# Performance work log

Measured on AMD Instinct MI355X. Metric: run time of the kernel, lower is better.

## Reference

```python
import jax, jax.numpy as jnp
import numpy as np
from jax import lax
from jax.scipy.special import logsumexp

NUM_CLASSES = 170
ALPHA = 0.2
B, T = 16, 8192


def setup_inputs() -> dict:
    key = jax.random.key(0)
    logits = jax.random.normal(key, (B, T, NUM_CLASSES), dtype=jnp.float32)
    # transition matrix: alpha on diagonal, uniform off-diagonal
    off = (1.0 - ALPHA) / (NUM_CLASSES - 1)
    trans = jnp.full((NUM_CLASSES, NUM_CLASSES), off, dtype=jnp.float32)
    trans = trans.at[jnp.arange(NUM_CLASSES), jnp.arange(NUM_CLASSES)].set(ALPHA)
    init = jnp.full((NUM_CLASSES,), 1.0 / NUM_CLASSES, dtype=jnp.float32)
    return {"logits": logits, "transition_matrix": trans, "initial_distribution": init}


def reference(logits, transition_matrix, initial_distribution):
    eps = 1e-12
    log_T = jnp.log(transition_matrix + eps)          # (C, C)
    log_init = jnp.log(initial_distribution + eps)    # (C,)
    log_probs = jax.nn.log_softmax(logits, axis=-1)   # (B, T, C)
    Bn, Tn, C = log_probs.shape
    lp = jnp.moveaxis(log_probs, 1, 0)                # (T, B, C) time-major for scan

    # forward recursion: alpha_t[j] = logsumexp_i(alpha_{t-1}[i] + logT[i,j]) + lp_t[j]
    alpha0 = log_init[None, :] + lp[0]                # (B, C)

    def fwd_step(a_prev, lp_t):
        a = logsumexp(a_prev[:, :, None] + log_T[None, :, :], axis=1) + lp_t
        return a, a

    _, alpha_rest = lax.scan(fwd_step, alpha0, lp[1:])
    alpha = jnp.concatenate([alpha0[None], alpha_rest], axis=0)  # (T, B, C)

    # backward recursion: beta_t[i] = logsumexp_j(logT[i,j] + lp_{t+1}[j] + beta_{t+1}[j])
    betaT = jnp.zeros((Bn, C), dtype=log_probs.dtype)

    def bwd_step(b_next, lp_next):
        b = logsumexp(log_T[None, :, :] + (lp_next + b_next)[:, None, :], axis=2)
        return b, b

    _, beta_rest = lax.scan(bwd_step, betaT, lp[1:], reverse=True)
    beta = jnp.concatenate([beta_rest, betaT[None]], axis=0)     # (T, B, C)

    posterior = jax.nn.softmax(alpha + beta, axis=-1)            # (T, B, C)
    return jnp.moveaxis(posterior, 0, 1)                         # (B, T, C)
```

## Files before the change

kernel.cpp:

```cpp
#include <hip/hip_runtime.h>
#include <hip/hip_fp16.h>


#define NCLS 170
#define BB 16
#define TT 8192
#define LCH 16
#define WARM 16
#define NCHUNK (TT / LCH)

typedef float f32x2 __attribute__((ext_vector_type(2)));

struct Row { f32x2 xy; float z; };

__device__ __forceinline__ float wave_sum_b(float x) {
  x += __int_as_float(__builtin_amdgcn_update_dpp(0, __float_as_int(x), 0x111, 0xF, 0xF, true));
  x += __int_as_float(__builtin_amdgcn_update_dpp(0, __float_as_int(x), 0x112, 0xF, 0xF, true));
  x += __int_as_float(__builtin_amdgcn_update_dpp(0, __float_as_int(x), 0x114, 0xF, 0xF, true));
  x += __int_as_float(__builtin_amdgcn_update_dpp(0, __float_as_int(x), 0x118, 0xF, 0xF, true));
  x += __int_as_float(__builtin_amdgcn_update_dpp(0, __float_as_int(x), 0x142, 0xA, 0xF, true));
  x += __int_as_float(__builtin_amdgcn_update_dpp(0, __float_as_int(x), 0x143, 0xC, 0xF, true));
  return __int_as_float(__builtin_amdgcn_readlane(__float_as_int(x), 63));
}

__global__ __launch_bounds__(256, 2) void hmm_fb(const float* __restrict__ logits,
                                                 const float* __restrict__ trans,
                                                 const float* __restrict__ initd,
                                                 float* __restrict__ out) {
  __shared__ __half2 pb01[4 * LCH * 64];
  const int lane = threadIdx.x & 63;
  const int w = threadIdx.x >> 6;
  __half2* pw = pb01 + w * (LCH * 64);

  const int d = blockIdx.x;
  const int o = (d & 7) * (BB * NCHUNK / 32) + (d >> 3);
  const int g = o * 4 + w;
  const int b = g / NCHUNK;
  const int chunk = g % NCHUNK;
  const int t0 = chunk * LCH;
  const int t1 = t0 + LCH;

  const float off = trans[1] + 1e-12f;
  const float dia = trans[0] + 1e-12f;
  const float dd = dia - off;
  const f32x2 dd2 = {dd, dd};

  const bool cok = (lane < NCLS - 128);
  const float* lg = logits + (size_t)b * TT * NCLS;

  auto ldraw = [&](int t) -> Row {
    const float* r = lg + (size_t)t * NCLS;
    Row wv;
    wv.xy = *(const f32x2*)(r + 2 * lane);
    wv.z = cok ? r[128 + lane] : 0.f;
    return wv;
  };
  auto eRow = [&](const Row& wv) -> Row {
    Row e;
    e.xy.x = __expf(wv.xy.x);
    e.xy.y = __expf(wv.xy.y);
    e.z = cok ? __expf(wv.z) : 0.f;
    return e;
  };

  __half2 ph2[LCH / 2];

  f32x2 v01; float v2s;
  auto fcore = [&](const Row& e, f32x2& u01, float& u2) -> float {
    u01 = v01 * e.xy;
    u2 = v2s * e.z;
    float S = wave_sum_b(u01.x + u01.y + u2);
    float os = off * S;
    f32x2 os2 = {os, os};
    v01 = dd2 * u01 + os2;
    v2s = __fmaf_rn(dd, u2, os);
    return S;
  };

  Row a0, a1, a2, a3, b0, b1, b2, b3;
  int ts;
  if (t0 == 0) {
    ts = 0;
    v01 = *(const f32x2*)(initd + 2 * lane);
    v2s = cok ? initd[128 + lane] : 0.f;
  } else {
    ts = t0 - WARM;
    v01.x = 1.f; v01.y = 1.f; v2s = cok ? 1.f : 0.f;
  }
  a0 = ldraw(ts); a1 = ldraw(ts + 1); a2 = ldraw(ts + 2); a3 = ldraw(ts + 3);
  b0 = ldraw(ts + 4); b1 = ldraw(ts + 5); b2 = ldraw(ts + 6); b3 = ldraw(ts + 7);

  for (int gg = 0; gg < (t0 - ts) / 4; ++gg) {
    const int tn = ts + 8 + 4 * gg;
    Row n0 = ldraw(tn), n1 = ldraw(tn + 1), n2 = ldraw(tn + 2), n3 = ldraw(tn + 3);
    Row e0 = eRow(a0), e1 = eRow(a1), e2 = eRow(a2), e3 = eRow(a3);
    f32x2 u01; float u2;
    fcore(e0, u01, u2);
    fcore(e1, u01, u2);
    fcore(e2, u01, u2);
    float S3 = fcore(e3, u01, u2);
    float rs = __builtin_amdgcn_rcpf(S3);
    f32x2 rs2 = {rs, rs};
    v01 = v01 * rs2; v2s *= rs;
    a0 = b0; a1 = b1; a2 = b2; a3 = b3;
    b0 = n0; b1 = n1; b2 = n2; b3 = n3;
  }

#define FGROUP(i)                                                              \
  {                                                                            \
    const int tn = t0 + (i) + 8;                                               \
    Row n0 = ldraw(tn + 0 > t1 - 1 ? t1 - 1 : tn + 0);                         \
    Row n1 = ldraw(tn + 1 > t1 - 1 ? t1 - 1 : tn + 1);                         \
    Row n2 = ldraw(tn + 2 > t1 - 1 ? t1 - 1 : tn + 2);                         \
    Row n3 = ldraw(tn + 3 > t1 - 1 ? t1 - 1 : tn + 3);                         \
    Row e0 = eRow(a0), e1 = eRow(a1), e2 = eRow(a2), e3 = eRow(a3);            \
    f32x2 u01; float u2;                                                       \
    float S0 = fcore(e0, u01, u2);                                             \
    float x0 = __builtin_amdgcn_rcpf(S0);                                      \
    pw[((i) + 0) * 64 + lane] = __floats2half2_rn(u01.x * x0, u01.y * x0);     \
    __half pa = __float2half(u2 * x0);                                         \
    float S1 = fcore(e1, u01, u2);                                             \
    float x1 = __builtin_amdgcn_rcpf(S1);                                      \
    pw[((i) + 1) * 64 + lane] = __floats2half2_rn(u01.x * x1, u01.y * x1);     \
    ph2[(i) / 2] = __halves2half2(pa, __float2half(u2 * x1));                  \
    float S2 = fcore(e2, u01, u2);                                             \
    float x2 = __builtin_amdgcn_rcpf(S2);                                      \
    pw[((i) + 2) * 64 + lane] = __floats2half2_rn(u01.x * x2, u01.y * x2);     \
    __half pb = __float2half(u2 * x2);                                         \
    float S3 = fcore(e3, u01, u2);                                             \
    float x3 = __builtin_amdgcn_rcpf(S3);                                      \
    pw[((i) + 3) * 64 + lane] = __floats2half2_rn(u01.x * x3, u01.y * x3);     \
    ph2[(i) / 2 + 1] = __halves2half2(pb, __float2half(u2 * x3));              \
    f32x2 x32 = {x3, x3};                                                      \
    v01 = v01 * x32; v2s *= x3;             \
    a0 = b0; a1 = b1; a2 = b2; a3 = b3;                                        \
    b0 = n0; b1 = n1; b2 = n2; b3 = n3;                                        \
  }

  FGROUP(0) FGROUP(4) FGROUP(8) FGROUP(12)
#undef FGROUP

  f32x2 q01; q01.x = 1.f; q01.y = 1.f;
  float q2 = cok ? 1.f : 0.f;
  int te2 = t1 + WARM;
  if (te2 > TT) te2 = TT;
  const int tstart = te2 - 1;

  auto ldB = [&](int tp1) -> Row {
    int rr = tp1 < 0 ? 0 : (tp1 > TT - 1 ? TT - 1 : tp1);
    Row wv = ldraw(rr);
    if (tp1 >= TT) { wv.xy.x = 0.f; wv.xy.y = 0.f; wv.z = 0.f; }
    return wv;
  };
  auto bcore = [&](const Row& e) -> float {
    f32x2 w01 = e.xy * q01;
    float w2 = e.z * q2;
    float S = wave_sum_b(w01.x + w01.y + w2);
    float os = off * S;
    f32x2 os2 = {os, os};
    q01 = dd2 * w01 + os2;
    q2 = __fmaf_rn(dd, w2, os);
    return S;
  };

  a0 = ldB(tstart + 1); a1 = ldB(tstart); a2 = ldB(tstart - 1); a3 = ldB(tstart - 2);
  b0 = ldB(tstart - 3); b1 = ldB(tstart - 4); b2 = ldB(tstart - 5); b3 = ldB(tstart - 6);

  for (int gg = 0; gg < (te2 - t1) / 4; ++gg) {
    const int tp = tstart - 7 - 4 * gg;
    Row n0 = ldB(tp), n1 = ldB(tp - 1), n2 = ldB(tp - 2), n3 = ldB(tp - 3);
    Row e0 = eRow(a0), e1 = eRow(a1), e2 = eRow(a2), e3 = eRow(a3);
    bcore(e0); bcore(e1); bcore(e2);
    float S3 = bcore(e3);
    float rs = __builtin_amdgcn_rcpf(S3);
    f32x2 rs2 = {rs, rs};
    q01 = q01 * rs2; q2 *= rs;
    a0 = b0; a1 = b1; a2 = b2; a3 = b3;
    b0 = n0; b1 = n1; b2 = n2; b3 = n3;
  }

#define WPOST(tt, ta)                                                          \
  {                                                                            \
    __half2 h01 = pw[(tt) * 64 + lane];                                        \
    f32x2 p01; p01.x = __low2float(h01); p01.y = __high2float(h01);            \
    f32x2 a01 = p01 * q01;                                                     \
    __half2 h2v = ph2[(tt) >> 1];                                              \
    float p2f = ((tt) & 1) ? __high2float(h2v) : __low2float(h2v);             \
    float g2 = cok ? p2f * q2 : 0.f;                                           \
    float z = wave_sum_b(a01.x + a01.y + g2);                                  \
    float iz = __builtin_amdgcn_rcpf(z);                                       \
    f32x2 iz2 = {iz, iz};                                                      \
    float* op = out + ((size_t)b * TT + (ta)) * NCLS;                          \
    f32x2 o01 = a01 * iz2;                                                     \
    __builtin_nontemporal_store(o01, (f32x2*)(op + 2 * lane));                 \
    if (cok) __builtin_nontemporal_store(g2 * iz, op + 128 + lane);            \
  }

#define BGROUP(i)                                                              \
  {                                                                            \
    const int tp = t1 - 8 - (i);                  \
    Row n0 = ldB(tp + 0 < t0 + 1 ? t0 + 1 : tp + 0);                           \
    Row n1 = ldB(tp - 1 < t0 + 1 ? t0 + 1 : tp - 1);                           \
    Row n2 = ldB(tp - 2 < t0 + 1 ? t0 + 1 : tp - 2);                           \
    Row n3 = ldB(tp - 3 < t0 + 1 ? t0 + 1 : tp - 3);                           \
    Row e0 = eRow(a0), e1 = eRow(a1), e2 = eRow(a2), e3 = eRow(a3);            \
    const int t = t1 - 1 - (i);                                                \
    bcore(e0); WPOST(LCH - 1 - (i), t)                                         \
    bcore(e1); WPOST(LCH - 2 - (i), t - 1)                                     \
    bcore(e2); WPOST(LCH - 3 - (i), t - 2)                                     \
    float S3 = bcore(e3); WPOST(LCH - 4 - (i), t - 3)                          \
    float rs = __builtin_amdgcn_rcpf(S3);                                      \
    f32x2 rs2 = {rs, rs};                                                      \
    q01 = q01 * rs2; q2 *= rs;                                                 \
    a0 = b0; a1 = b1; a2 = b2; a3 = b3;                                        \
    b0 = n0; b1 = n1; b2 = n2; b3 = n3;                                        \
  }

  BGROUP(0) BGROUP(4) BGROUP(8) BGROUP(12)
#undef BGROUP
#undef WPOST
}

extern "C" void kernel_launch(void* const* d_in, const int* in_sizes, int n_in,
                              void* d_out, int out_size, void* d_ws, size_t ws_size,
                              hipStream_t stream) {
  const float* logits = (const float*)d_in[0];
  const float* trans  = (const float*)d_in[1];
  const float* initd  = (const float*)d_in[2];
  float* out = (float*)d_out;
  dim3 grid(BB * NCHUNK / 4);
  dim3 block(256);
  hipLaunchKernelGGL(hmm_fb, grid, block, 0, stream, logits, trans, initd, out);
}
```

Before: 61.46 us.

## Split forward and backward recursions across two waves per chunk of 32 steps

Each block now handles one chunk of 32 timesteps with two waves. Wave 0 runs the forward warmup and the forward pass and stores the scaled forward values to shared memory. Wave 1 meanwhile runs the backward warmup, then after a barrier does the backward pass and writes the posterior. This overlaps the backward warmup with the forward pass and halves the warmup overhead per timestep by doubling the chunk length. The cost is an idle wave during the second phase and a serial forward-then-backward dependency per block.

```diff
diff --git a/kernel.cpp b/kernel.cpp
--- a/kernel.cpp
+++ b/kernel.cpp
@@ -5,9 +5,10 @@
 #define NCLS 170
 #define BB 16
 #define TT 8192
-#define LCH 16
+#define LCH 32
 #define WARM 16
 #define NCHUNK (TT / LCH)
+#define P2S 44
 
 typedef float f32x2 __attribute__((ext_vector_type(2)));
 
@@ -23,20 +24,19 @@
   return __int_as_float(__builtin_amdgcn_readlane(__float_as_int(x), 63));
 }
 
-__global__ __launch_bounds__(256, 2) void hmm_fb(const float* __restrict__ logits,
+__global__ __launch_bounds__(128, 4) void hmm_fb(const float* __restrict__ logits,
                                                  const float* __restrict__ trans,
                                                  const float* __restrict__ initd,
                                                  float* __restrict__ out) {
-  __shared__ __half2 pb01[4 * LCH * 64];
+  __shared__ __half2 p01[LCH * 64];
+  __shared__ __half  p2s[LCH * P2S];
   const int lane = threadIdx.x & 63;
   const int w = threadIdx.x >> 6;
-  __half2* pw = pb01 + w * (LCH * 64);
 
   const int d = blockIdx.x;
-  const int o = (d & 7) * (BB * NCHUNK / 32) + (d >> 3);
-  const int g = o * 4 + w;
-  const int b = g / NCHUNK;
-  const int chunk = g % NCHUNK;
+  const int o = (d & 7) * (BB * NCHUNK / 8) + (d >> 3);
+  const int b = o / NCHUNK;
+  const int chunk = o % NCHUNK;
   const int t0 = chunk * LCH;
   const int t1 = t0 + LCH;
 
@@ -63,48 +63,61 @@
     return e;
   };
 
-  __half2 ph2[LCH / 2];
-
-  f32x2 v01; float v2s;
-  auto fcore = [&](const Row& e, f32x2& u01, float& u2) -> float {
-    u01 = v01 * e.xy;
-    u2 = v2s * e.z;
-    float S = wave_sum_b(u01.x + u01.y + u2);
-    float os = off * S;
-    f32x2 os2 = {os, os};
-    v01 = dd2 * u01 + os2;
-    v2s = __fmaf_rn(dd, u2, os);
-    return S;
+  Row a0, a1, a2, a3, b0, b1, b2, b3;
+  f32x2 q01 = {1.f, 1.f};
+  float q2 = cok ? 1.f : 0.f;
+
+  auto ldB = [&](int tp1) -> Row {
+    int rr = tp1 < 0 ? 0 : (tp1 > TT - 1 ? TT - 1 : tp1);
+    Row wv = ldraw(rr);
+    if (tp1 >= TT) { wv.xy.x = 0.f; wv.xy.y = 0.f; wv.z = 0.f; }
+    return wv;
   };
 
-  Row a0, a1, a2, a3, b0, b1, b2, b3;
-  int ts;
-  if (t0 == 0) {
-    ts = 0;
-    v01 = *(const f32x2*)(initd + 2 * lane);
-    v2s = cok ? initd[128 + lane] : 0.f;
-  } else {
-    ts = t0 - WARM;
-    v01.x = 1.f; v01.y = 1.f; v2s = cok ? 1.f : 0.f;
-  }
-  a0 = ldraw(ts); a1 = ldraw(ts + 1); a2 = ldraw(ts + 2); a3 = ldraw(ts + 3);
-  b0 = ldraw(ts + 4); b1 = ldraw(ts + 5); b2 = ldraw(ts + 6); b3 = ldraw(ts + 7);
-
-  for (int gg = 0; gg < (t0 - ts) / 4; ++gg) {
-    const int tn = ts + 8 + 4 * gg;
-    Row n0 = ldraw(tn), n1 = ldraw(tn + 1), n2 = ldraw(tn + 2), n3 = ldraw(tn + 3);
-    Row e0 = eRow(a0), e1 = eRow(a1), e2 = eRow(a2), e3 = eRow(a3);
-    f32x2 u01; float u2;
-    fcore(e0, u01, u2);
-    fcore(e1, u01, u2);
-    fcore(e2, u01, u2);
-    float S3 = fcore(e3, u01, u2);
-    float rs = __builtin_amdgcn_rcpf(S3);
-    f32x2 rs2 = {rs, rs};
-    v01 = v01 * rs2; v2s *= rs;
-    a0 = b0; a1 = b1; a2 = b2; a3 = b3;
-    b0 = n0; b1 = n1; b2 = n2; b3 = n3;
-  }
+  if (w == 0) {
+    f32x2 v01; float v2s;
+    auto fcore = [&](const Row& e, f32x2& u01, float& u2) -> float {
+      u01 = v01 * e.xy;
+      u2 = v2s * e.z;
+      float S = wave_sum_b(u01.x + u01.y + u2);
+      float os = off * S;
+      f32x2 os2 = {os, os};
+      v01 = dd2 * u01 + os2;
+      v2s = __fmaf_rn(dd, u2, os);
+      return S;
+    };
+
+    int ts;
+    if (t0 == 0) {
+      ts = 0;
+      v01 = *(const f32x2*)(initd + 2 * lane);
+      v2s = cok ? initd[128 + lane] : 0.f;
+    } else {
+      ts = t0 - WARM;
+      v01.x = 1.f; v01.y = 1.f; v2s = cok ? 1.f : 0.f;
+    }
+    a0 = ldraw(ts); a1 = ldraw(ts + 1); a2 = ldraw(ts + 2); a3 = ldraw(ts + 3);
+    b0 = ldraw(ts + 4); b1 = ldraw(ts + 5); b2 = ldraw(ts + 6); b3 = ldraw(ts + 7);
+
+    for (int gg = 0; gg < (t0 - ts) / 4; ++gg) {
+      const int tn = ts + 8 + 4 * gg;
+      Row n0 = ldraw(tn), n1 = ldraw(tn + 1), n2 = ldraw(tn + 2), n3 = ldraw(tn + 3);
+      Row e0 = eRow(a0), e1 = eRow(a1), e2 = eRow(a2), e3 = eRow(a3);
+      f32x2 u01; float u2;
+      fcore(e0, u01, u2);
+      fcore(e1, u01, u2);
+      fcore(e2, u01, u2);
+      float S3 = fcore(e3, u01, u2);
+      float rs = __builtin_amdgcn_rcpf(S3);
+      f32x2 rs2 = {rs, rs};
+      v01 = v01 * rs2; v2s *= rs;
+      a0 = b0; a1 = b1; a2 = b2; a3 = b3;
+      b0 = n0; b1 = n1; b2 = n2; b3 = n3;
+    }
+
+#define FSTORE(st, u01v, u2v, xr)                                              \
+    p01[(st) * 64 + lane] = __floats2half2_rn(u01v.x * xr, u01v.y * xr);       \
+    if (cok) p2s[(st) * P2S + lane] = __float2half(u2v * xr);
 
 #define FGROUP(i)                                                              \
   {                                                                            \
@@ -117,76 +130,81 @@
     f32x2 u01; float u2;                                                       \
     float S0 = fcore(e0, u01, u2);                                             \
     float x0 = __builtin_amdgcn_rcpf(S0);                                      \
-    pw[((i) + 0) * 64 + lane] = __floats2half2_rn(u01.x * x0, u01.y * x0);     \
-    __half pa = __float2half(u2 * x0);                                         \
+    FSTORE((i) + 0, u01, u2, x0)                                               \
     float S1 = fcore(e1, u01, u2);                                             \
     float x1 = __builtin_amdgcn_rcpf(S1);                                      \
-    pw[((i) + 1) * 64 + lane] = __floats2half2_rn(u01.x * x1, u01.y * x1);     \
-    ph2[(i) / 2] = __halves2half2(pa, __float2half(u2 * x1));                  \
+    FSTORE((i) + 1, u01, u2, x1)                                               \
     float S2 = fcore(e2, u01, u2);                                             \
     float x2 = __builtin_amdgcn_rcpf(S2);                                      \
-    pw[((i) + 2) * 64 + lane] = __floats2half2_rn(u01.x * x2, u01.y * x2);     \
-    __half pb = __float2half(u2 * x2);                                         \
+    FSTORE((i) + 2, u01, u2, x2)                                               \
     float S3 = fcore(e3, u01, u2);                                             \
     float x3 = __builtin_amdgcn_rcpf(S3);                                      \
-    pw[((i) + 3) * 64 + lane] = __floats2half2_rn(u01.x * x3, u01.y * x3);     \
-    ph2[(i) / 2 + 1] = __halves2half2(pb, __float2half(u2 * x3));              \
+    FSTORE((i) + 3, u01, u2, x3)                                               \
     f32x2 x32 = {x3, x3};                                                      \
     v01 = v01 * x32; v2s *= x3;             \
     a0 = b0; a1 = b1; a2 = b2; a3 = b3;                                        \
     b0 = n0; b1 = n1; b2 = n2; b3 = n3;                                        \
   }
 
-  FGROUP(0) FGROUP(4) FGROUP(8) FGROUP(12)
+    FGROUP(0) FGROUP(4) FGROUP(8) FGROUP(12)
+    FGROUP(16) FGROUP(20) FGROUP(24) FGROUP(28)
 #undef FGROUP
-
-  f32x2 q01; q01.x = 1.f; q01.y = 1.f;
-  float q2 = cok ? 1.f : 0.f;
-  int te2 = t1 + WARM;
-  if (te2 > TT) te2 = TT;
-  const int tstart = te2 - 1;
-
-  auto ldB = [&](int tp1) -> Row {
-    int rr = tp1 < 0 ? 0 : (tp1 > TT - 1 ? TT - 1 : tp1);
-    Row wv = ldraw(rr);
-    if (tp1 >= TT) { wv.xy.x = 0.f; wv.xy.y = 0.f; wv.z = 0.f; }
-    return wv;
-  };
-  auto bcore = [&](const Row& e) -> float {
-    f32x2 w01 = e.xy * q01;
-    float w2 = e.z * q2;
-    float S = wave_sum_b(w01.x + w01.y + w2);
-    float os = off * S;
-    f32x2 os2 = {os, os};
-    q01 = dd2 * w01 + os2;
-    q2 = __fmaf_rn(dd, w2, os);
-    return S;
-  };
-
-  a0 = ldB(tstart + 1); a1 = ldB(tstart); a2 = ldB(tstart - 1); a3 = ldB(tstart - 2);
-  b0 = ldB(tstart - 3); b1 = ldB(tstart - 4); b2 = ldB(tstart - 5); b3 = ldB(tstart - 6);
-
-  for (int gg = 0; gg < (te2 - t1) / 4; ++gg) {
-    const int tp = tstart - 7 - 4 * gg;
-    Row n0 = ldB(tp), n1 = ldB(tp - 1), n2 = ldB(tp - 2), n3 = ldB(tp - 3);
-    Row e0 = eRow(a0), e1 = eRow(a1), e2 = eRow(a2), e3 = eRow(a3);
-    bcore(e0); bcore(e1); bcore(e2);
-    float S3 = bcore(e3);
-    float rs = __builtin_amdgcn_rcpf(S3);
-    f32x2 rs2 = {rs, rs};
-    q01 = q01 * rs2; q2 *= rs;
-    a0 = b0; a1 = b1; a2 = b2; a3 = b3;
-    b0 = n0; b1 = n1; b2 = n2; b3 = n3;
-  }
+#undef FSTORE
+  } else {
+    auto bcore = [&](const Row& e) -> float {
+      f32x2 w01 = e.xy * q01;
+      float w2 = e.z * q2;
+      float S = wave_sum_b(w01.x + w01.y + w2);
+      float os = off * S;
+      f32x2 os2 = {os, os};
+      q01 = dd2 * w01 + os2;
+      q2 = __fmaf_rn(dd, w2, os);
+      return S;
+    };
+
+    int te2 = t1 + WARM;
+    if (te2 > TT) te2 = TT;
+    const int tstart = te2 - 1;
+
+    a0 = ldB(tstart + 1); a1 = ldB(tstart); a2 = ldB(tstart - 1); a3 = ldB(tstart - 2);
+    b0 = ldB(tstart - 3); b1 = ldB(tstart - 4); b2 = ldB(tstart - 5); b3 = ldB(tstart - 6);
+
+    for (int gg = 0; gg < (te2 - t1) / 4; ++gg) {
+      const int tp = tstart - 7 - 4 * gg;
+      Row n0 = ldB(tp), n1 = ldB(tp - 1), n2 = ldB(tp - 2), n3 = ldB(tp - 3);
+      Row e0 = eRow(a0), e1 = eRow(a1), e2 = eRow(a2), e3 = eRow(a3);
+      bcore(e0); bcore(e1); bcore(e2);
+      float S3 = bcore(e3);
+      float rs = __builtin_amdgcn_rcpf(S3);
+      f32x2 rs2 = {rs, rs};
+      q01 = q01 * rs2; q2 *= rs;
+      a0 = b0; a1 = b1; a2 = b2; a3 = b3;
+      b0 = n0; b1 = n1; b2 = n2; b3 = n3;
+    }
+  }
+
+  __syncthreads();
+
+  if (w == 1) {
+    auto bcore = [&](const Row& e) -> float {
+      f32x2 w01 = e.xy * q01;
+      float w2 = e.z * q2;
+      float S = wave_sum_b(w01.x + w01.y + w2);
+      float os = off * S;
+      f32x2 os2 = {os, os};
+      q01 = dd2 * w01 + os2;
+      q2 = __fmaf_rn(dd, w2, os);
+      return S;
+    };
 
 #define WPOST(tt, ta)                                                          \
   {                                                                            \
-    __half2 h01 = pw[(tt) * 64 + lane];                                        \
-    f32x2 p01; p01.x = __low2float(h01); p01.y = __high2float(h01);            \
-    f32x2 a01 = p01 * q01;                                                     \
-    __half2 h2v = ph2[(tt) >> 1];                                              \
-    float p2f = ((tt) & 1) ? __high2float(h2v) : __low2float(h2v);             \
-    float g2 = cok ? p2f * q2 : 0.f;                                           \
+    __half2 h01 = p01[(tt) * 64 + lane];                                       \
+    f32x2 p01v; p01v.x = __low2float(h01); p01v.y = __high2float(h01);         \
+    f32x2 a01 = p01v * q01;                                                    \
+    float p2f = 0.f;                                                           \
+    if (cok) p2f = __half2float(p2s[(tt) * P2S + lane]);                       \
+    float g2 = p2f * q2;                                                       \
     float z = wave_sum_b(a01.x + a01.y + g2);                                  \
     float iz = __builtin_amdgcn_rcpf(z);                                       \
     f32x2 iz2 = {iz, iz};                                                      \
@@ -216,9 +234,11 @@
     b0 = n0; b1 = n1; b2 = n2; b3 = n3;                                        \
   }
 
-  BGROUP(0) BGROUP(4) BGROUP(8) BGROUP(12)
+    BGROUP(0) BGROUP(4) BGROUP(8) BGROUP(12)
+    BGROUP(16) BGROUP(20) BGROUP(24) BGROUP(28)
 #undef BGROUP
 #undef WPOST
+  }
 }
 
 extern "C" void kernel_launch(void* const* d_in, const int* in_sizes, int n_in,
@@ -228,7 +248,7 @@
   const float* trans  = (const float*)d_in[1];
   const float* initd  = (const float*)d_in[2];
   float* out = (float*)d_out;
-  dim3 grid(BB * NCHUNK / 4);
-  dim3 block(256);
+  dim3 grid(BB * NCHUNK);
+  dim3 block(128);
   hipLaunchKernelGGL(hmm_fb, grid, block, 0, stream, logits, trans, initd, out);
 }
```

Result: slower. 71.77 us (+16.8%).
